# Performance work log

Hardware: AMD Instinct MI355X
Metric: run time of the kernel (lower is better)

Reference implementation:

```python
import jax, jax.numpy as jnp
import numpy as np

B, L, D, H, NL, FF, W, V = 4, 8192, 256, 4, 4, 1024, 512, 14
DH = D // H


def _ln(x, g, b, eps=1e-5):
    m = jnp.mean(x, axis=-1, keepdims=True)
    v = jnp.mean((x - m) ** 2, axis=-1, keepdims=True)
    return (x - m) / jnp.sqrt(v + eps) * g + b


def setup_inputs() -> dict:
    key = jax.random.key(0)
    ks = jax.random.split(key, 12)
    s = 0.02
    inp = {
        "byte_ids": jax.random.randint(ks[0], (B, L), 0, V, dtype=jnp.int32),
        "embed": jax.random.normal(ks[1], (V, D), jnp.float32) * s,
        "wq": jax.random.normal(ks[2], (NL, D, D), jnp.float32) * s,
        "bq": jnp.zeros((NL, D), jnp.float32),
        "wk": jax.random.normal(ks[3], (NL, D, D), jnp.float32) * s,
        "bk": jnp.zeros((NL, D), jnp.float32),
        "wv": jax.random.normal(ks[4], (NL, D, D), jnp.float32) * s,
        "bv": jnp.zeros((NL, D), jnp.float32),
        "wo": jax.random.normal(ks[5], (NL, D, D), jnp.float32) * s,
        "bo": jnp.zeros((NL, D), jnp.float32),
        "ln1_g": jnp.ones((NL, D), jnp.float32),
        "ln1_b": jnp.zeros((NL, D), jnp.float32),
        "ln2_g": jnp.ones((NL, D), jnp.float32),
        "ln2_b": jnp.zeros((NL, D), jnp.float32),
        "w1": jax.random.normal(ks[6], (NL, D, FF), jnp.float32) * s,
        "b1": jnp.zeros((NL, FF), jnp.float32),
        "w2": jax.random.normal(ks[7], (NL, FF, D), jnp.float32) * s,
        "b2": jnp.zeros((NL, D), jnp.float32),
        "lnf_g": jnp.ones((D,), jnp.float32),
        "lnf_b": jnp.zeros((D,), jnp.float32),
        "head_w": jax.random.normal(ks[8], (D, V), jnp.float32) * s,
    }
    return inp


def _forward(byte_ids, embed, wq, bq, wk, bk, wv, bv, wo, bo,
             ln1_g, ln1_b, ln2_g, ln2_b, w1, b1, w2, b2, lnf_g, lnf_b, head_w):
    x = embed[byte_ids]                      # [B, L, D]
    nb = L // W                              # number of 512-wide blocks
    scale = 1.0 / np.sqrt(DH)
    # ALiBi slopes: 2^(-8h/H) for h = 1..H
    slopes = jnp.exp2(-8.0 * jnp.arange(1, H + 1, dtype=jnp.float32) / H)
    qi = jnp.arange(W)[:, None]
    ki = jnp.arange(2 * W)[None, :]
    dist = (W + qi - ki).astype(jnp.float32)            # i - j for kv window [prev, cur]
    base = (dist >= 0) & (dist <= W)                    # causal sliding window (left=512)
    mask = jnp.broadcast_to(base, (nb, W, 2 * W))
    mask = mask.at[0].set(base & (ki >= W))             # first block has no previous block
    bias = -slopes[:, None, None] * dist                # [H, W, 2W]

    for l in range(NL):
        h = _ln(x, ln1_g[l], ln1_b[l])
        q = (h @ wq[l] + bq[l]).reshape(B, nb, W, H, DH)
        k = (h @ wk[l] + bk[l]).reshape(B, nb, W, H, DH)
        v = (h @ wv[l] + bv[l]).reshape(B, nb, W, H, DH)
        kp = jnp.pad(k, ((0, 0), (1, 0), (0, 0), (0, 0), (0, 0)))[:, :nb]
        vp = jnp.pad(v, ((0, 0), (1, 0), (0, 0), (0, 0), (0, 0)))[:, :nb]
        kk = jnp.concatenate([kp, k], axis=2)           # [B, nb, 2W, H, DH]
        vv = jnp.concatenate([vp, v], axis=2)
        s = jnp.einsum('bnqhd,bnkhd->bhnqk', q, kk) * scale + bias[None, :, None]
        s = jnp.where(mask[None, None], s, -1e9)
        p = jax.nn.softmax(s, axis=-1)                  # [B, H, nb, W, 2W]
        o = jnp.einsum('bhnqk,bnkhd->bnqhd', p, vv).reshape(B, L, D)
        x = x + o @ wo[l] + bo[l]
        h2 = _ln(x, ln2_g[l], ln2_b[l])
        x = x + jax.nn.gelu(h2 @ w1[l] + b1[l]) @ w2[l] + b2[l]
    x = _ln(x, lnf_g, lnf_b)
    return x @ head_w                                   # [B, L, V]


def reference(byte_ids, embed, wq, bq, wk, bk, wv, bv, wo, bo,
              ln1_g, ln1_b, ln2_g, ln2_b, w1, b1, w2, b2, lnf_g, lnf_b, head_w):
    return _forward(byte_ids, embed, wq, bq, wk, bk, wv, bv, wo, bo,
                    ln1_g, ln1_b, ln2_g, ln2_b, w1, b1, w2, b2, lnf_g, lnf_b, head_w)
```

## Files before the change

kernel.cpp:

```cpp
#include <hip/hip_runtime.h>

#define NLAYER 4
#define M_TOK 32768

typedef unsigned short u16;
typedef __bf16 bf16x8 __attribute__((ext_vector_type(8)));
typedef float f32x4 __attribute__((ext_vector_type(4)));

__device__ inline float bf2f(u16 u) {
    union { unsigned int i; float f; } x; x.i = ((unsigned int)u) << 16; return x.f;
}
__device__ inline u16 f2bf(float f) {
    union { float f; unsigned int i; } x; x.f = f;
    return (u16)((x.i + 0x8000u) >> 16);
}
__device__ inline bf16x8 ld_frag(const u16* p) {
    union { uint4 u; bf16x8 b; } c; c.u = *(const uint4*)p; return c.b;
}
__device__ inline unsigned pk2(float a, float b) {
    union { float f; unsigned i; } ua, ub; ua.f = a; ub.f = b;
    return __builtin_amdgcn_perm(ub.i + 0x8000u, ua.i + 0x8000u, 0x07060302u);
}
__device__ inline float gelu_f(float x) {
    float z = 0.7978845608028654f * (x + 0.044715f * x * x * x);
    float t = 1.f - 2.f / (__expf(2.f * z) + 1.f);
    return 0.5f * x * (1.f + t);
}
__device__ inline void gload_lds16(const u16* g, u16* l) {
    __builtin_amdgcn_global_load_lds(
        (const __attribute__((address_space(1))) unsigned int*)g,
        (__attribute__((address_space(3))) unsigned int*)l, 16, 0, 0);
}

#define BAR()   asm volatile("s_barrier" ::: "memory")
#define WAIT4() asm volatile("s_waitcnt vmcnt(4)" ::: "memory")
#define WAIT0() asm volatile("s_waitcnt vmcnt(0)" ::: "memory")
#define LGKM0() asm volatile("s_waitcnt lgkmcnt(0)" ::: "memory")

__global__ void sniff_kernel(const u16* __restrict__ raw, int* __restrict__ flag)
{
    if (threadIdx.x == 0 && blockIdx.x == 0) {
        int ok = 1;
        for (int i = 0; i < 32; i++) {
            u16 u = raw[i];
            int e = (u >> 7) & 0xFF;
            if (!(u == 0 || (e >= 90 && e <= 140))) ok = 0;
        }
        *flag = ok;
    }
}

struct IngestArgs { const void* src[20]; int off[21]; };
__global__ __launch_bounds__(256) void ingest_all(
    IngestArgs a, float* __restrict__ dst, const int* __restrict__ flag, int tot)
{
    int gid = blockIdx.x * 256 + threadIdx.x;
    if (gid >= tot) return;
    int lo = 0, hi = 20;
    while (hi - lo > 1) { int mid = (lo + hi) >> 1; if (gid >= a.off[mid]) lo = mid; else hi = mid; }
    int local = gid - a.off[lo];
    if (*flag) dst[gid] = bf2f(((const u16*)a.src[lo])[local]);
    else       dst[gid] = ((const float*)a.src[lo])[local];
}

__global__ __launch_bounds__(256) void pack_qkv(
    const float* __restrict__ wq, const float* __restrict__ wk, const float* __restrict__ wv,
    const float* __restrict__ bq, const float* __restrict__ bk, const float* __restrict__ bv,
    u16* __restrict__ wT, float* __restrict__ bT)
{
    int l = blockIdx.y;
    int idx = blockIdx.x * 256 + threadIdx.x;
    int n = idx >> 8, k = idx & 255;
    const float* w = (n < 256) ? wq : (n < 512) ? wk : wv;
    int nn = n & 255;
    wT[(size_t)l * 768 * 256 + idx] = f2bf(w[(size_t)l * 65536 + k * 256 + nn]);
    if (idx < 768) {
        const float* bb = (idx < 256) ? bq : (idx < 512) ? bk : bv;
        bT[l * 768 + idx] = bb[l * 256 + (idx & 255)];
    }
}

__global__ __launch_bounds__(256) void pack_t(
    const float* __restrict__ src, u16* __restrict__ dst, int R, int C)
{
    int l = blockIdx.y;
    int idx = blockIdx.x * 256 + threadIdx.x;
    int c = idx / R, r = idx % R;
    size_t base = (size_t)l * R * C;
    dst[base + idx] = f2bf(src[base + (size_t)r * C + c]);
}

__global__ __launch_bounds__(256) void embed_kernel(
    const int* __restrict__ ids, const float* __restrict__ emb, float* __restrict__ x)
{
    int t = blockIdx.x * 256 + threadIdx.x;
    int row = t >> 6, c = (t & 63) * 4;
    int id = ids[row];
    float4 e = *(const float4*)(emb + (size_t)id * 256 + c);
    *(float4*)(x + (size_t)row * 256 + c) = e;
}

__global__ __launch_bounds__(256) void ln_kernel(
    const float* __restrict__ x, const float* __restrict__ g, const float* __restrict__ b,
    u16* __restrict__ out)
{
    int row = blockIdx.x * 4 + (threadIdx.x >> 6);
    int lane = threadIdx.x & 63;
    float4 v = *(const float4*)(x + (size_t)row * 256 + lane * 4);
    float s = v.x + v.y + v.z + v.w;
    float s2 = v.x * v.x + v.y * v.y + v.z * v.z + v.w * v.w;
    #pragma unroll
    for (int mk = 1; mk < 64; mk <<= 1) {
        s += __shfl_xor(s, mk, 64);
        s2 += __shfl_xor(s2, mk, 64);
    }
    float mean = s * (1.f / 256.f);
    float var = s2 * (1.f / 256.f) - mean * mean;
    float rstd = rsqrtf(var + 1e-5f);
    int d0 = lane * 4;
    float4 gg = *(const float4*)(g + d0);
    float4 bb = *(const float4*)(b + d0);
    union { unsigned long long u; u16 q[4]; } oo;
    oo.q[0] = f2bf((v.x - mean) * rstd * gg.x + bb.x);
    oo.q[1] = f2bf((v.y - mean) * rstd * gg.y + bb.y);
    oo.q[2] = f2bf((v.z - mean) * rstd * gg.z + bb.z);
    oo.q[3] = f2bf((v.w - mean) * rstd * gg.w + bb.w);
    *(unsigned long long*)(out + (size_t)row * 256 + d0) = oo.u;
}

template <int EPI, int K>
__global__ __launch_bounds__(256, 3) void gemm_db(
    const u16* __restrict__ A, const u16* __restrict__ Bt, const float* __restrict__ bias,
    u16* __restrict__ outB, float* __restrict__ resid, int N)
{
    __shared__ u16 lds[17408];
    constexpr int NC = K / 32;
    int tid = threadIdx.x, lane = tid & 63, wave = tid >> 6;
    int col = lane & 15, quad = lane >> 4;
    int wm = (wave >> 1) * 64, wn = (wave & 1) * 64;
    int bm = blockIdx.x * 128, bn = blockIdx.y * 128;

    u16* A0 = lds;          u16* A1 = lds + 4096;
    u16* B0 = lds + 8192;   u16* B1 = lds + 12288;

    int rL = wave * 32 + (lane >> 2);
    int sx = (lane & 3) ^ ((lane >> 2) & 3);
    const u16* srcA0 = A + (size_t)(bm + rL) * K + sx * 8;
    const u16* srcB0 = Bt + (size_t)(bn + rL) * K + sx * 8;
    int st = wave * 1024 + lane * 8;

    int g8 = (quad ^ (col & 3)) * 8;
    int aoff = (wm + col) * 32 + g8;
    int boff = (wn + col) * 32 + g8;

    f32x4 z4 = { 0.f, 0.f, 0.f, 0.f };
    f32x4 acc[4][4];
    #pragma unroll
    for (int i = 0; i < 4; i++)
        #pragma unroll
        for (int j = 0; j < 4; j++) acc[i][j] = z4;

    #define STAGE(c, Ax, Bx) do {                                        \
        const u16* _a = srcA0 + (c) * 32;                                \
        const u16* _b = srcB0 + (c) * 32;                                \
        gload_lds16(_a, (Ax) + st);                                      \
        gload_lds16(_a + (size_t)16 * K, (Ax) + st + 512);               \
        gload_lds16(_b, (Bx) + st);                                      \
        gload_lds16(_b + (size_t)16 * K, (Bx) + st + 512);               \
    } while (0)

    #define CHUNK(Ax, Bx) do {                                           \
        bf16x8 af[4], bfv[4];                                            \
        _Pragma("unroll")                                                \
        for (int i = 0; i < 4; i++) af[i] = ld_frag((Ax) + aoff + i * 512); \
        _Pragma("unroll")                                                \
        for (int j = 0; j < 4; j++) bfv[j] = ld_frag((Bx) + boff + j * 512); \
        _Pragma("unroll")                                                \
        for (int i = 0; i < 4; i++)                                      \
            _Pragma("unroll")                                            \
            for (int j = 0; j < 4; j++)                                  \
                acc[i][j] = __builtin_amdgcn_mfma_f32_16x16x32_bf16(af[i], bfv[j], acc[i][j], 0, 0, 0); \
    } while (0)

    STAGE(0, A0, B0);
    for (int c = 0; c < NC - 2; c += 2) {
        STAGE(c + 1, A1, B1);
        WAIT4(); BAR();
        CHUNK(A0, B0);
        LGKM0(); BAR();
        STAGE(c + 2, A0, B0);
        WAIT4(); BAR();
        CHUNK(A1, B1);
        LGKM0(); BAR();
    }
    STAGE(NC - 1, A1, B1);
    WAIT4(); BAR();
    CHUNK(A0, B0);
    LGKM0(); BAR();
    WAIT0(); BAR();
    CHUNK(A1, B1);
    __syncthreads();

    if (EPI == 2) {
        float* Cf = (float*)lds;
        #pragma unroll
        for (int h = 0; h < 2; h++) {
            if ((wave & 1) == h) {
                #pragma unroll
                for (int j = 0; j < 4; j++) {
                    float bv = bias[bn + wn + j * 16 + col];
                    #pragma unroll
                    for (int i = 0; i < 4; i++) {
                        int rl = wm + i * 16 + quad * 4;
                        #pragma unroll
                        for (int r = 0; r < 4; r++)
                            Cf[(rl + r) * 68 + j * 16 + col] = acc[i][j][r] + bv;
                    }
                }
            }
            LGKM0(); BAR();
            #pragma unroll
            for (int u = 0; u < 8; u++) {
                int row = u * 16 + (tid >> 4);
                int cseg = (tid & 15) * 4;
                float* rp = resid + (size_t)(bm + row) * N + bn + h * 64 + cseg;
                const float* cp = Cf + row * 68 + cseg;
                float4 rv = *(float4*)rp;
                float4 cv = *(const float4*)cp;
                rv.x += cv.x; rv.y += cv.y; rv.z += cv.z; rv.w += cv.w;
                *(float4*)rp = rv;
            }
            LGKM0(); BAR();
        }
    } else {
        u16* Cs = lds;
        #pragma unroll
        for (int j = 0; j < 4; j++) {
            int ccl = wn + j * 16 + col;
            float bv = bias[bn + ccl];
            #pragma unroll
            for (int i = 0; i < 4; i++) {
                int rl = wm + i * 16 + quad * 4;
                #pragma unroll
                for (int r = 0; r < 4; r++) {
                    float v = acc[i][j][r] + bv;
                    if (EPI == 1) v = gelu_f(v);
                    Cs[(rl + r) * 136 + ccl] = f2bf(v);
                }
            }
        }
        __syncthreads();
        #pragma unroll
        for (int u = 0; u < 8; u++) {
            int row = u * 16 + (tid >> 4);
            int c8 = (tid & 15) * 8;
            u16* op = outB + (size_t)(bm + row) * N + bn + c8;
            *(uint4*)op = *(const uint4*)(Cs + row * 136 + c8);
        }
    }
    #undef STAGE
    #undef CHUNK
}

__global__ __launch_bounds__(512, 2) void mlp2(
    const float* __restrict__ xin, const u16* __restrict__ w1T, const u16* __restrict__ w2T,
    const float* __restrict__ gamma, const float* __restrict__ beta,
    const float* __restrict__ b1, const float* __restrict__ b2, float* __restrict__ xr)
{
    __shared__ u16 L[72704];
    int tid = threadIdx.x, lane = tid & 63, wave = tid >> 6;
    int col = lane & 15, quad = lane >> 4;
    int g8 = (quad ^ (col & 3)) * 8;
    int bm = blockIdx.x * 128;

    {
        int sub = tid & 7, rsel = tid >> 3;
        float4 g4[8], b4[8];
        #pragma unroll
        for (int q = 0; q < 8; q++) {
            g4[q] = *(const float4*)(gamma + sub * 32 + q * 4);
            b4[q] = *(const float4*)(beta  + sub * 32 + q * 4);
        }
        #pragma unroll
        for (int p = 0; p < 2; p++) {
            int row = p * 64 + rsel;
            const float* xp = xin + (size_t)(bm + row) * 256 + sub * 32;
            float4 v4[8];
            #pragma unroll
            for (int q = 0; q < 8; q++) v4[q] = *(const float4*)(xp + q * 4);
            float s1 = 0.f, s2 = 0.f;
            #pragma unroll
            for (int q = 0; q < 8; q++) {
                s1 += v4[q].x + v4[q].y + v4[q].z + v4[q].w;
                s2 += v4[q].x * v4[q].x + v4[q].y * v4[q].y
                    + v4[q].z * v4[q].z + v4[q].w * v4[q].w;
            }
            s1 += __shfl_xor(s1, 1, 64); s2 += __shfl_xor(s2, 1, 64);
            s1 += __shfl_xor(s1, 2, 64); s2 += __shfl_xor(s2, 2, 64);
            s1 += __shfl_xor(s1, 4, 64); s2 += __shfl_xor(s2, 4, 64);
            float mean = s1 * (1.f / 256.f);
            float var  = s2 * (1.f / 256.f) - mean * mean;
            float rstd = rsqrtf(var + 1e-5f);
            #pragma unroll
            for (int j = 0; j < 4; j++) {
                float4 a = v4[2 * j], c = v4[2 * j + 1];
                float4 ga = g4[2 * j], gc = g4[2 * j + 1];
                float4 ba = b4[2 * j], bc = b4[2 * j + 1];
                union { uint4 u; u16 q[8]; } pkv;
                pkv.q[0] = f2bf((a.x - mean) * rstd * ga.x + ba.x);
                pkv.q[1] = f2bf((a.y - mean) * rstd * ga.y + ba.y);
                pkv.q[2] = f2bf((a.z - mean) * rstd * ga.z + ba.z);
                pkv.q[3] = f2bf((a.w - mean) * rstd * ga.w + ba.w);
                pkv.q[4] = f2bf((c.x - mean) * rstd * gc.x + bc.x);
                pkv.q[5] = f2bf((c.y - mean) * rstd * gc.y + bc.y);
                pkv.q[6] = f2bf((c.z - mean) * rstd * gc.z + bc.z);
                pkv.q[7] = f2bf((c.w - mean) * rstd * gc.w + bc.w);
                *(uint4*)(L + sub * 4096 + row * 32 + ((j ^ (row & 3)) * 8)) = pkv.u;
            }
        }
        float2 bv = *(const float2*)(b1 + tid * 2);
        *(float2*)((float*)(L + 70656) + tid * 2) = bv;
    }

    #define STAGE_W1(ff, base) do {                                                  \
        _Pragma("unroll")                                                            \
        for (int gg = 0; gg < 2; gg++) {                                             \
            int u_ = gg * 512 + tid;                                                 \
            int ks_ = u_ >> 7, rowf_ = (u_ & 127) >> 2, s_ = u_ & 3;                 \
            gload_lds16(w1T + (size_t)((ff) * 32 + rowf_) * 256 + ks_ * 32           \
                            + ((s_ ^ (rowf_ & 3)) * 8),                              \
                        L + (base) + u_ * 8);                                        \
        }                                                                            \
    } while (0)

    #define STAGE_W2(ff, base) do {                                                  \
        _Pragma("unroll")                                                            \
        for (int gg = 0; gg < 2; gg++) {                                             \
            int u_ = gg * 512 + tid;                                                 \
            int d_ = u_ >> 2, s_ = u_ & 3;                                           \
            gload_lds16(w2T + (size_t)d_ * 1024 + (ff) * 32 + ((s_ ^ (d_ & 3)) * 8), \
                        L + (base) + u_ * 8);                                        \
        }                                                                            \
    } while (0)

    STAGE_W1(0, 32768);
    STAGE_W2(0, 49152);
    WAIT0(); LGKM0(); BAR();

    f32x4 z4 = { 0.f, 0.f, 0.f, 0.f };
    f32x4 acc2[16];
    #pragma unroll
    for (int n = 0; n < 16; n++) acc2[n] = z4;
    u16* Gw = L + 65536 + wave * 640;
    const float* b1l = (const float*)(L + 70656);
    int aoffB = (wave * 16 + col) * 32 + g8;

    #pragma unroll 2
    for (int f = 0; f < 32; ++f) {
        int pc = f & 1, pn = pc ^ 1;
        if (f < 31) {
            STAGE_W1(f + 1, 32768 + pn * 8192);
            STAGE_W2(f + 1, 49152 + pn * 8192);
            WAIT4();
        } else WAIT0();
        BAR();

        const u16* w1b = L + 32768 + pc * 8192;
        const u16* w2b = L + 49152 + pc * 8192;

        f32x4 a1[2]; a1[0] = z4; a1[1] = z4;
        #pragma unroll
        for (int ks = 0; ks < 8; ks++) {
            bf16x8 hf = ld_frag(L + ks * 4096 + aoffB);
            #pragma unroll
            for (int kt = 0; kt < 2; kt++) {
                bf16x8 wf = ld_frag(w1b + ks * 1024 + (kt * 16 + col) * 32 + g8);
                a1[kt] = __builtin_amdgcn_mfma_f32_16x16x32_bf16(wf, hf, a1[kt], 0, 0, 0);
            }
        }
        #pragma unroll
        for (int kt = 0; kt < 2; kt++) {
            float4 bv = *(const float4*)(b1l + f * 32 + kt * 16 + quad * 4);
            float p0 = gelu_f(a1[kt][0] + bv.x);
            float p1 = gelu_f(a1[kt][1] + bv.y);
            float p2 = gelu_f(a1[kt][2] + bv.z);
            float p3 = gelu_f(a1[kt][3] + bv.w);
            uint2 w; w.x = pk2(p0, p1); w.y = pk2(p2, p3);
            *(uint2*)(Gw + col * 40 + kt * 16 + quad * 4) = w;
        }
        LGKM0();

        bf16x8 gf = ld_frag(Gw + col * 40 + quad * 8);
        #pragma unroll
        for (int nt = 0; nt < 16; nt++) {
            bf16x8 wf2 = ld_frag(w2b + (nt * 16 + col) * 32 + g8);
            acc2[nt] = __builtin_amdgcn_mfma_f32_16x16x32_bf16(gf, wf2, acc2[nt], 0, 0, 0);
        }
        LGKM0(); BAR();
    }

    float b2v[16];
    #pragma unroll
    for (int nt = 0; nt < 16; nt++) b2v[nt] = b2[nt * 16 + col];
    #pragma unroll
    for (int nt = 0; nt < 16; nt++) {
        #pragma unroll
        for (int r = 0; r < 4; r++) {
            float* p = xr + (size_t)(bm + wave * 16 + quad * 4 + r) * 256 + nt * 16 + col;
            *p += acc2[nt][r] + b2v[nt];
        }
    }
    #undef STAGE_W1
    #undef STAGE_W2
}

__global__ __launch_bounds__(256, 3) void attn_kernel(
    const u16* __restrict__ qkv, u16* __restrict__ attno)
{
    __shared__ u16 Ks[64 * 72];
    __shared__ u16 Vt[64 * 68];
    __shared__ u16 Ps[4 * 16 * 72];
    int g = blockIdx.x;
    int xc = g & 7, t = g >> 3;
    int r12 = t & 15, s8 = t >> 4;
    int ng = s8 * 8 + xc;
    int bb = ng >> 4, nn = ng & 15;
    int hh = r12 & 3, t2 = r12 >> 2;
    int tid = threadIdx.x, lane = tid & 63, wave = tid >> 6;
    int q16 = lane & 15, quad = lane >> 4;
    float slope = exp2f(-2.f * (float)(hh + 1));
    float slopeL = slope * 1.44269504f;
    const float C1 = 0.125f * 1.44269504f;

    int qt0 = t2 * 2;
    size_t tok0 = (size_t)bb * 8192 + nn * 512;

    bf16x8 bqf[2][2];
    {
        int qrow = t2 * 128 + wave * 16 + q16;
        const u16* qp = qkv + (tok0 + qrow) * 768 + hh * 64 + quad * 8;
        bqf[0][0] = ld_frag(qp);
        bqf[0][1] = ld_frag(qp + 32);
        const u16* qp1 = qp + (size_t)64 * 768;
        bqf[1][0] = ld_frag(qp1);
        bqf[1][1] = ld_frag(qp1 + 32);
    }

    f32x4 z4 = { 0.f, 0.f, 0.f, 0.f };
    f32x4 oa[2][4];
    #pragma unroll
    for (int s = 0; s < 2; s++)
        #pragma unroll
        for (int dt = 0; dt < 4; dt++) oa[s][dt] = z4;
    float lsum[2] = { 0.f, 0.f };
    u16* Psw = Ps + wave * (16 * 72);

    int c_lo = (nn == 0) ? 8 : qt0;
    int c_hi = qt0 + 9;

    int kkK = tid >> 3, c8k = (tid & 7) * 8;
    int kk2 = (tid & 31) * 2, c8v = (tid >> 5) * 8;

    uint4 pk0, pk1, pv0, pv1;
    auto load_c = [&](int c) {
        int tok = (int)tok0 - 512 + c * 64;
        const u16* bK = qkv + (size_t)(tok + kkK) * 768 + hh * 64 + 256 + c8k;
        pk0 = *(const uint4*)bK;
        pk1 = *(const uint4*)(bK + (size_t)32 * 768);
        const u16* bV = qkv + (size_t)(tok + kk2) * 768 + hh * 64 + 512 + c8v;
        pv0 = *(const uint4*)bV;
        pv1 = *(const uint4*)(bV + 768);
    };
    load_c(c_lo);

    for (int c = c_lo; c <= c_hi; ++c) {
        LGKM0(); BAR();
        *(uint4*)(Ks + kkK * 72 + c8k) = pk0;
        *(uint4*)(Ks + (kkK + 32) * 72 + c8k) = pk1;
        {
            union { uint4 u; u16 s[8]; } a, b;
            a.u = pv0; b.u = pv1;
            #pragma unroll
            for (int j = 0; j < 8; j++) {
                unsigned w = (unsigned)a.s[j] | ((unsigned)b.s[j] << 16);
                *(unsigned*)(Vt + (c8v + j) * 68 + kk2) = w;
            }
        }
        if (c < c_hi) load_c(c + 1);
        LGKM0(); BAR();

        bf16x8 kf[4][2];
        #pragma unroll
        for (int kt = 0; kt < 4; kt++)
            #pragma unroll
            for (int ks = 0; ks < 2; ks++)
                kf[kt][ks] = ld_frag(Ks + (kt * 16 + q16) * 72 + ks * 32 + quad * 8);
        bf16x8 vf[4][2];
        #pragma unroll
        for (int dt = 0; dt < 4; dt++)
            #pragma unroll
            for (int ks = 0; ks < 2; ks++) {
                union { uint2 p[2]; bf16x8 b; } cv;
                const u16* vp = Vt + (dt * 16 + q16) * 68 + ks * 32 + quad * 8;
                cv.p[0] = *(const uint2*)(vp);
                cv.p[1] = *(const uint2*)(vp + 4);
                vf[dt][ks] = cv.b;
            }

        int act0 = (c <= qt0 + 8);
        int act1 = (c >= qt0 + 1);
        #pragma unroll
        for (int s = 0; s < 2; s++) {
            if (s == 0 ? !act0 : !act1) continue;
            f32x4 st[4];
            #pragma unroll
            for (int kt = 0; kt < 4; kt++) {
                f32x4 z = z4;
                #pragma unroll
                for (int ks = 0; ks < 2; ks++)
                    z = __builtin_amdgcn_mfma_f32_16x16x32_bf16(kf[kt][ks], bqf[s][ks], z, 0, 0, 0);
                st[kt] = z;
            }
            int qg = t2 * 128 + s * 64 + wave * 16 + q16;
            int D = 512 + qg - c * 64 - quad * 4;
            float nb = -slopeL * (float)D;
            int qts = qt0 + s;
            int diag = (c == qts) || (c == qts + 8);
            float ls = 0.f;
            #pragma unroll
            for (int kt = 0; kt < 4; kt++) {
                float pk[4];
                #pragma unroll
                for (int r = 0; r < 4; r++) {
                    float bias = fmaf(slopeL, (float)(kt * 16 + r), nb);
                    float p = exp2f(fmaf(st[kt][r], C1, bias));
                    if (diag) {
                        int dd = D - (kt * 16 + r);
                        p = ((unsigned)dd <= 512u) ? p : 0.f;
                    }
                    ls += p; pk[r] = p;
                }
                uint2 w;
                w.x = pk2(pk[0], pk[1]);
                w.y = pk2(pk[2], pk[3]);
                *(uint2*)(Psw + q16 * 72 + kt * 16 + quad * 4) = w;
            }
            lsum[s] += ls;
            bf16x8 pf[2];
            #pragma unroll
            for (int ks = 0; ks < 2; ks++)
                pf[ks] = ld_frag(Psw + q16 * 72 + ks * 32 + quad * 8);
            #pragma unroll
            for (int dt = 0; dt < 4; dt++)
                #pragma unroll
                for (int ks = 0; ks < 2; ks++)
                    oa[s][dt] = __builtin_amdgcn_mfma_f32_16x16x32_bf16(pf[ks], vf[dt][ks], oa[s][dt], 0, 0, 0);
        }
    }

    #pragma unroll
    for (int s = 0; s < 2; s++) {
        float lr = lsum[s];
        lr += __shfl_xor(lr, 16, 64);
        lr += __shfl_xor(lr, 32, 64);
        lsum[s] = lr;
    }
    float* lx = (float*)Psw;
    if (quad == 0) { lx[q16] = lsum[0]; lx[16 + q16] = lsum[1]; }
    #pragma unroll
    for (int s = 0; s < 2; s++) {
        float4 lq = *(const float4*)(lx + s * 16 + quad * 4);
        float inv[4] = { 1.f / lq.x, 1.f / lq.y, 1.f / lq.z, 1.f / lq.w };
        int tokb = (int)tok0 + t2 * 128 + s * 64 + wave * 16 + quad * 4;
        #pragma unroll
        for (int r = 0; r < 4; r++)
            #pragma unroll
            for (int dt = 0; dt < 4; dt++)
                attno[(size_t)(tokb + r) * 256 + hh * 64 + dt * 16 + q16] = f2bf(oa[s][dt][r] * inv[r]);
    }
}

__global__ __launch_bounds__(256) void head_ln_kernel(
    const float* __restrict__ x, const float* __restrict__ g, const float* __restrict__ b,
    const float* __restrict__ hw, const int* __restrict__ flag,
    u16* __restrict__ outb, float* __restrict__ outf)
{
    __shared__ float Wt[14 * 256];
    int tid = threadIdx.x;
    for (int i = tid; i < 14 * 256; i += 256) {
        int v = i >> 8, d = i & 255;
        Wt[i] = hw[d * 14 + v];
    }
    __syncthreads();
    int wave = tid >> 6, lane = tid & 63;
    int row = blockIdx.x * 4 + wave;
    float4 v = *(const float4*)(x + (size_t)row * 256 + lane * 4);
    float s = v.x + v.y + v.z + v.w;
    float s2 = v.x * v.x + v.y * v.y + v.z * v.z + v.w * v.w;
    #pragma unroll
    for (int mk = 1; mk < 64; mk <<= 1) {
        s += __shfl_xor(s, mk, 64);
        s2 += __shfl_xor(s2, mk, 64);
    }
    float mean = s * (1.f / 256.f);
    float var = s2 * (1.f / 256.f) - mean * mean;
    float rstd = rsqrtf(var + 1e-5f);
    int d0 = lane * 4;
    float4 gg = *(const float4*)(g + d0);
    float4 bb = *(const float4*)(b + d0);
    float hv[4];
    hv[0] = (v.x - mean) * rstd * gg.x + bb.x;
    hv[1] = (v.y - mean) * rstd * gg.y + bb.y;
    hv[2] = (v.z - mean) * rstd * gg.z + bb.z;
    hv[3] = (v.w - mean) * rstd * gg.w + bb.w;
    int isbf = *flag;
    for (int vv = 0; vv < 14; vv++) {
        float4 wv4 = *(const float4*)(Wt + vv * 256 + lane * 4);
        float sd = hv[0] * wv4.x + hv[1] * wv4.y + hv[2] * wv4.z + hv[3] * wv4.w;
        #pragma unroll
        for (int mk = 1; mk < 64; mk <<= 1) sd += __shfl_xor(sd, mk, 64);
        if (lane == 0) {
            if (isbf) outb[(size_t)row * 14 + vv] = f2bf(sd);
            else      outf[(size_t)row * 14 + vv] = sd;
        }
    }
}

extern "C" void kernel_launch(void* const* d_in, const int* in_sizes, int n_in,
                              void* d_out, int out_size, void* d_ws, size_t ws_size,
                              hipStream_t stream) {
    (void)out_size; (void)ws_size;
    const int* ids = (const int*)d_in[0];

    char* ws = (char*)d_ws;
    int* flag = (int*)ws; ws += 16;

    IngestArgs ia;
    int off = 0;
    for (int i = 1; i < n_in && i <= 20; i++) {
        ia.src[i - 1] = d_in[i];
        ia.off[i - 1] = off;
        off += in_sizes[i];
    }
    ia.off[20] = off;
    float* fbase = (float*)ws;
    ws += (size_t)((off + 3) & ~3) * 4;
    float* fin[21];
    for (int i = 1; i <= 20; i++) fin[i] = fbase + ia.off[i - 1];

    float* x    = (float*)ws;  ws += (size_t)M_TOK * 256 * 4;
    u16* h      = (u16*)ws;    ws += (size_t)M_TOK * 256 * 2;
    u16* qkv    = (u16*)ws;    ws += (size_t)M_TOK * 768 * 2;
    u16* attno  = (u16*)ws;    ws += (size_t)M_TOK * 256 * 2;
    u16* wqkvT  = (u16*)ws;    ws += (size_t)NLAYER * 768 * 256 * 2;
    u16* woT    = (u16*)ws;    ws += (size_t)NLAYER * 256 * 256 * 2;
    u16* w1T    = (u16*)ws;    ws += (size_t)NLAYER * 1024 * 256 * 2;
    u16* w2T    = (u16*)ws;    ws += (size_t)NLAYER * 256 * 1024 * 2;
    float* bqkv = (float*)ws;  ws += (size_t)NLAYER * 768 * 4;

    sniff_kernel<<<1, 64, 0, stream>>>((const u16*)d_in[1], flag);
    ingest_all<<<(off + 255) / 256, 256, 0, stream>>>(ia, fbase, flag, off);

    pack_qkv<<<dim3(768, NLAYER), 256, 0, stream>>>(fin[2], fin[4], fin[6],
                                                    fin[3], fin[5], fin[7], wqkvT, bqkv);
    pack_t<<<dim3(256, NLAYER), 256, 0, stream>>>(fin[8], woT, 256, 256);
    pack_t<<<dim3(1024, NLAYER), 256, 0, stream>>>(fin[14], w1T, 256, 1024);
    pack_t<<<dim3(1024, NLAYER), 256, 0, stream>>>(fin[16], w2T, 1024, 256);

    embed_kernel<<<8192, 256, 0, stream>>>(ids, fin[1], x);

    for (int l = 0; l < NLAYER; ++l) {
        ln_kernel<<<8192, 256, 0, stream>>>(x, fin[10] + l * 256, fin[11] + l * 256, h);
        gemm_db<0, 256><<<dim3(256, 6), 256, 0, stream>>>(h, wqkvT + (size_t)l * 768 * 256,
                                                          bqkv + l * 768, qkv, nullptr, 768);
        attn_kernel<<<1024, 256, 0, stream>>>(qkv, attno);
        gemm_db<2, 256><<<dim3(256, 2), 256, 0, stream>>>(attno, woT + (size_t)l * 65536,
                                                          fin[9] + l * 256, nullptr, x, 256);
        mlp2<<<256, 512, 0, stream>>>(x, w1T + (size_t)l * 262144,
                                      w2T + (size_t)l * 262144,
                                      fin[12] + l * 256, fin[13] + l * 256,
                                      fin[15] + l * 1024, fin[17] + l * 256, x);
    }
    head_ln_kernel<<<8192, 256, 0, stream>>>(x, fin[18], fin[19], fin[20], flag,
                                             (u16*)d_out, (float*)d_out);
}
```

Before: 1.000 ms.

## Split MLP into producer/consumer waves and fuse next-layer LayerNorm into epilogue

The fused MLP kernel now gives the first four waves the W1 GEMM plus GELU, each over 32 rows. The other four waves run the W2 GEMM one step behind on a double-buffered G tile in LDS, with W2 staging shifted to match. The residual epilogue also computes the next layer's LayerNorm and writes the bf16 h. That removes the standalone ln_kernel launches, and the embed kernel fuses the first LN. The costs are more LDS, more accumulator registers per consumer wave, and idle producer waves during the epilogue.

Result: faster. 978.5 us (-2.2%).

```diff
diff --git a/kernel.cpp b/kernel.cpp
--- a/kernel.cpp
+++ b/kernel.cpp
@@ -34,6 +34,7 @@
 
 #define BAR()   asm volatile("s_barrier" ::: "memory")
 #define WAIT4() asm volatile("s_waitcnt vmcnt(4)" ::: "memory")
+#define WAIT2() asm volatile("s_waitcnt vmcnt(2)" ::: "memory")
 #define WAIT0() asm volatile("s_waitcnt vmcnt(0)" ::: "memory")
 #define LGKM0() asm volatile("s_waitcnt lgkmcnt(0)" ::: "memory")
 
@@ -90,25 +91,18 @@
     dst[base + idx] = f2bf(src[base + (size_t)r * C + c]);
 }
 
-__global__ __launch_bounds__(256) void embed_kernel(
-    const int* __restrict__ ids, const float* __restrict__ emb, float* __restrict__ x)
+__global__ __launch_bounds__(256) void embed_ln(
+    const int* __restrict__ ids, const float* __restrict__ emb,
+    const float* __restrict__ g, const float* __restrict__ b,
+    float* __restrict__ x, u16* __restrict__ h)
 {
     int t = blockIdx.x * 256 + threadIdx.x;
     int row = t >> 6, c = (t & 63) * 4;
     int id = ids[row];
     float4 e = *(const float4*)(emb + (size_t)id * 256 + c);
     *(float4*)(x + (size_t)row * 256 + c) = e;
-}
-
-__global__ __launch_bounds__(256) void ln_kernel(
-    const float* __restrict__ x, const float* __restrict__ g, const float* __restrict__ b,
-    u16* __restrict__ out)
-{
-    int row = blockIdx.x * 4 + (threadIdx.x >> 6);
-    int lane = threadIdx.x & 63;
-    float4 v = *(const float4*)(x + (size_t)row * 256 + lane * 4);
-    float s = v.x + v.y + v.z + v.w;
-    float s2 = v.x * v.x + v.y * v.y + v.z * v.z + v.w * v.w;
+    float s = e.x + e.y + e.z + e.w;
+    float s2 = e.x * e.x + e.y * e.y + e.z * e.z + e.w * e.w;
     #pragma unroll
     for (int mk = 1; mk < 64; mk <<= 1) {
         s += __shfl_xor(s, mk, 64);
@@ -117,15 +111,14 @@
     float mean = s * (1.f / 256.f);
     float var = s2 * (1.f / 256.f) - mean * mean;
     float rstd = rsqrtf(var + 1e-5f);
-    int d0 = lane * 4;
-    float4 gg = *(const float4*)(g + d0);
-    float4 bb = *(const float4*)(b + d0);
+    float4 gg = *(const float4*)(g + c);
+    float4 bb = *(const float4*)(b + c);
     union { unsigned long long u; u16 q[4]; } oo;
-    oo.q[0] = f2bf((v.x - mean) * rstd * gg.x + bb.x);
-    oo.q[1] = f2bf((v.y - mean) * rstd * gg.y + bb.y);
-    oo.q[2] = f2bf((v.z - mean) * rstd * gg.z + bb.z);
-    oo.q[3] = f2bf((v.w - mean) * rstd * gg.w + bb.w);
-    *(unsigned long long*)(out + (size_t)row * 256 + d0) = oo.u;
+    oo.q[0] = f2bf((e.x - mean) * rstd * gg.x + bb.x);
+    oo.q[1] = f2bf((e.y - mean) * rstd * gg.y + bb.y);
+    oo.q[2] = f2bf((e.z - mean) * rstd * gg.z + bb.z);
+    oo.q[3] = f2bf((e.w - mean) * rstd * gg.w + bb.w);
+    *(unsigned long long*)(h + (size_t)row * 256 + c) = oo.u;
 }
 
 template <int EPI, int K>
@@ -262,16 +255,20 @@
     #undef CHUNK
 }
 
-__global__ __launch_bounds__(512, 2) void mlp2(
+template <int FUSE>
+__global__ __launch_bounds__(512, 2) void mlp2s(
     const float* __restrict__ xin, const u16* __restrict__ w1T, const u16* __restrict__ w2T,
     const float* __restrict__ gamma, const float* __restrict__ beta,
-    const float* __restrict__ b1, const float* __restrict__ b2, float* __restrict__ xr)
-{
-    __shared__ u16 L[72704];
+    const float* __restrict__ b1, const float* __restrict__ b2, float* __restrict__ xr,
+    const float* __restrict__ g1n, const float* __restrict__ b1n, u16* __restrict__ hout)
+{
+    __shared__ u16 L[77824];
     int tid = threadIdx.x, lane = tid & 63, wave = tid >> 6;
     int col = lane & 15, quad = lane >> 4;
     int g8 = (quad ^ (col & 3)) * 8;
     int bm = blockIdx.x * 128;
+    int isProd = (wave < 4);
+    int pw = wave & 3;
 
     {
         int sub = tid & 7, rsel = tid >> 3;
@@ -319,7 +316,7 @@
             }
         }
         float2 bv = *(const float2*)(b1 + tid * 2);
-        *(float2*)((float*)(L + 70656) + tid * 2) = bv;
+        *(float2*)((float*)(L + 75776) + tid * 2) = bv;
     }
 
     #define STAGE_W1(ff, base) do {                                                  \
@@ -344,70 +341,122 @@
     } while (0)
 
     STAGE_W1(0, 32768);
-    STAGE_W2(0, 49152);
     WAIT0(); LGKM0(); BAR();
 
     f32x4 z4 = { 0.f, 0.f, 0.f, 0.f };
-    f32x4 acc2[16];
+    f32x4 acc2[2][16];
     #pragma unroll
-    for (int n = 0; n < 16; n++) acc2[n] = z4;
-    u16* Gw = L + 65536 + wave * 640;
-    const float* b1l = (const float*)(L + 70656);
-    int aoffB = (wave * 16 + col) * 32 + g8;
+    for (int mt = 0; mt < 2; mt++)
+        #pragma unroll
+        for (int nt = 0; nt < 16; nt++) acc2[mt][nt] = z4;
+    const float* b1l = (const float*)(L + 75776);
 
     #pragma unroll 2
     for (int f = 0; f < 32; ++f) {
         int pc = f & 1, pn = pc ^ 1;
-        if (f < 31) {
-            STAGE_W1(f + 1, 32768 + pn * 8192);
-            STAGE_W2(f + 1, 49152 + pn * 8192);
-            WAIT4();
-        } else WAIT0();
+        if (f < 31) STAGE_W1(f + 1, 32768 + pn * 8192);
+        STAGE_W2(f, 49152 + pc * 8192);
+        if (f == 31) WAIT2(); else WAIT4();
         BAR();
 
-        const u16* w1b = L + 32768 + pc * 8192;
-        const u16* w2b = L + 49152 + pc * 8192;
-
-        f32x4 a1[2]; a1[0] = z4; a1[1] = z4;
-        #pragma unroll
-        for (int ks = 0; ks < 8; ks++) {
-            bf16x8 hf = ld_frag(L + ks * 4096 + aoffB);
-            #pragma unroll
-            for (int kt = 0; kt < 2; kt++) {
-                bf16x8 wf = ld_frag(w1b + ks * 1024 + (kt * 16 + col) * 32 + g8);
-                a1[kt] = __builtin_amdgcn_mfma_f32_16x16x32_bf16(wf, hf, a1[kt], 0, 0, 0);
-            }
-        }
-        #pragma unroll
-        for (int kt = 0; kt < 2; kt++) {
-            float4 bv = *(const float4*)(b1l + f * 32 + kt * 16 + quad * 4);
-            float p0 = gelu_f(a1[kt][0] + bv.x);
-            float p1 = gelu_f(a1[kt][1] + bv.y);
-            float p2 = gelu_f(a1[kt][2] + bv.z);
-            float p3 = gelu_f(a1[kt][3] + bv.w);
-            uint2 w; w.x = pk2(p0, p1); w.y = pk2(p2, p3);
-            *(uint2*)(Gw + col * 40 + kt * 16 + quad * 4) = w;
-        }
-        LGKM0();
-
-        bf16x8 gf = ld_frag(Gw + col * 40 + quad * 8);
+        if (isProd) {
+            const u16* w1b = L + 32768 + pc * 8192;
+            f32x4 a1[2][2];
+            a1[0][0] = z4; a1[0][1] = z4; a1[1][0] = z4; a1[1][1] = z4;
+            #pragma unroll
+            for (int ks = 0; ks < 8; ks++) {
+                bf16x8 hf0 = ld_frag(L + ks * 4096 + (pw * 32 + col) * 32 + g8);
+                bf16x8 hf1 = ld_frag(L + ks * 4096 + (pw * 32 + 16 + col) * 32 + g8);
+                #pragma unroll
+                for (int kt = 0; kt < 2; kt++) {
+                    bf16x8 wf = ld_frag(w1b + ks * 1024 + (kt * 16 + col) * 32 + g8);
+                    a1[0][kt] = __builtin_amdgcn_mfma_f32_16x16x32_bf16(wf, hf0, a1[0][kt], 0, 0, 0);
+                    a1[1][kt] = __builtin_amdgcn_mfma_f32_16x16x32_bf16(wf, hf1, a1[1][kt], 0, 0, 0);
+                }
+            }
+            u16* gd = L + 65536 + pc * 5120;
+            #pragma unroll
+            for (int mt = 0; mt < 2; mt++)
+                #pragma unroll
+                for (int kt = 0; kt < 2; kt++) {
+                    float4 bv = *(const float4*)(b1l + f * 32 + kt * 16 + quad * 4);
+                    float p0 = gelu_f(a1[mt][kt][0] + bv.x);
+                    float p1 = gelu_f(a1[mt][kt][1] + bv.y);
+                    float p2 = gelu_f(a1[mt][kt][2] + bv.z);
+                    float p3 = gelu_f(a1[mt][kt][3] + bv.w);
+                    uint2 w; w.x = pk2(p0, p1); w.y = pk2(p2, p3);
+                    *(uint2*)(gd + (pw * 32 + mt * 16 + col) * 40 + kt * 16 + quad * 4) = w;
+                }
+        } else if (f > 0) {
+            const u16* gs = L + 65536 + pn * 5120;
+            const u16* w2b = L + 49152 + pn * 8192;
+            bf16x8 gf0 = ld_frag(gs + (pw * 32 + col) * 40 + quad * 8);
+            bf16x8 gf1 = ld_frag(gs + (pw * 32 + 16 + col) * 40 + quad * 8);
+            #pragma unroll
+            for (int nt = 0; nt < 16; nt++) {
+                bf16x8 wf2 = ld_frag(w2b + (nt * 16 + col) * 32 + g8);
+                acc2[0][nt] = __builtin_amdgcn_mfma_f32_16x16x32_bf16(gf0, wf2, acc2[0][nt], 0, 0, 0);
+                acc2[1][nt] = __builtin_amdgcn_mfma_f32_16x16x32_bf16(gf1, wf2, acc2[1][nt], 0, 0, 0);
+            }
+        }
+        LGKM0(); BAR();
+    }
+
+    WAIT0();
+    if (!isProd) {
+        const u16* gs = L + 65536 + 5120;
+        const u16* w2b = L + 49152 + 8192;
+        bf16x8 gf0 = ld_frag(gs + (pw * 32 + col) * 40 + quad * 8);
+        bf16x8 gf1 = ld_frag(gs + (pw * 32 + 16 + col) * 40 + quad * 8);
         #pragma unroll
         for (int nt = 0; nt < 16; nt++) {
             bf16x8 wf2 = ld_frag(w2b + (nt * 16 + col) * 32 + g8);
-            acc2[nt] = __builtin_amdgcn_mfma_f32_16x16x32_bf16(gf, wf2, acc2[nt], 0, 0, 0);
-        }
+            acc2[0][nt] = __builtin_amdgcn_mfma_f32_16x16x32_bf16(gf0, wf2, acc2[0][nt], 0, 0, 0);
+            acc2[1][nt] = __builtin_amdgcn_mfma_f32_16x16x32_bf16(gf1, wf2, acc2[1][nt], 0, 0, 0);
+        }
+
+        float b2v[16], g1v[16], b1v[16];
+        #pragma unroll
+        for (int nt = 0; nt < 16; nt++) {
+            b2v[nt] = b2[nt * 16 + col];
+            if (FUSE) { g1v[nt] = g1n[nt * 16 + col]; b1v[nt] = b1n[nt * 16 + col]; }
+        }
+        #pragma unroll
+        for (int mt = 0; mt < 2; mt++)
+            #pragma unroll
+            for (int r = 0; r < 4; r++) {
+                int m = pw * 32 + mt * 16 + quad * 4 + r;
+                float* xrow = xr + (size_t)(bm + m) * 256;
+                float s1 = 0.f, s2 = 0.f;
+                #pragma unroll
+                for (int nt = 0; nt < 16; nt++) {
+                    float xv = xrow[nt * 16 + col] + acc2[mt][nt][r] + b2v[nt];
+                    acc2[mt][nt][r] = xv;
+                    s1 += xv; s2 += xv * xv;
+                }
+                #pragma unroll
+                for (int nt = 0; nt < 16; nt++) xrow[nt * 16 + col] = acc2[mt][nt][r];
+                if (FUSE) {
+                    s1 += __shfl_xor(s1, 1, 64); s2 += __shfl_xor(s2, 1, 64);
+                    s1 += __shfl_xor(s1, 2, 64); s2 += __shfl_xor(s2, 2, 64);
+                    s1 += __shfl_xor(s1, 4, 64); s2 += __shfl_xor(s2, 4, 64);
+                    s1 += __shfl_xor(s1, 8, 64); s2 += __shfl_xor(s2, 8, 64);
+                    float mean = s1 * (1.f / 256.f);
+                    float var  = s2 * (1.f / 256.f) - mean * mean;
+                    float rstd = rsqrtf(var + 1e-5f);
+                    #pragma unroll
+                    for (int nt = 0; nt < 16; nt++)
+                        L[m * 256 + nt * 16 + col] =
+                            f2bf((acc2[mt][nt][r] - mean) * rstd * g1v[nt] + b1v[nt]);
+                }
+            }
+    }
+    if (FUSE) {
         LGKM0(); BAR();
-    }
-
-    float b2v[16];
-    #pragma unroll
-    for (int nt = 0; nt < 16; nt++) b2v[nt] = b2[nt * 16 + col];
-    #pragma unroll
-    for (int nt = 0; nt < 16; nt++) {
-        #pragma unroll
-        for (int r = 0; r < 4; r++) {
-            float* p = xr + (size_t)(bm + wave * 16 + quad * 4 + r) * 256 + nt * 16 + col;
-            *p += acc2[nt][r] + b2v[nt];
+        #pragma unroll
+        for (int i = 0; i < 8; i++) {
+            int flat = i * 4096 + tid * 8;
+            *(uint4*)(hout + (size_t)bm * 256 + flat) = *(const uint4*)(L + flat);
         }
     }
     #undef STAGE_W1
@@ -667,19 +716,27 @@
     pack_t<<<dim3(1024, NLAYER), 256, 0, stream>>>(fin[14], w1T, 256, 1024);
     pack_t<<<dim3(1024, NLAYER), 256, 0, stream>>>(fin[16], w2T, 1024, 256);
 
-    embed_kernel<<<8192, 256, 0, stream>>>(ids, fin[1], x);
+    embed_ln<<<8192, 256, 0, stream>>>(ids, fin[1], fin[10], fin[11], x, h);
 
     for (int l = 0; l < NLAYER; ++l) {
-        ln_kernel<<<8192, 256, 0, stream>>>(x, fin[10] + l * 256, fin[11] + l * 256, h);
         gemm_db<0, 256><<<dim3(256, 6), 256, 0, stream>>>(h, wqkvT + (size_t)l * 768 * 256,
                                                           bqkv + l * 768, qkv, nullptr, 768);
         attn_kernel<<<1024, 256, 0, stream>>>(qkv, attno);
         gemm_db<2, 256><<<dim3(256, 2), 256, 0, stream>>>(attno, woT + (size_t)l * 65536,
                                                           fin[9] + l * 256, nullptr, x, 256);
-        mlp2<<<256, 512, 0, stream>>>(x, w1T + (size_t)l * 262144,
-                                      w2T + (size_t)l * 262144,
-                                      fin[12] + l * 256, fin[13] + l * 256,
-                                      fin[15] + l * 1024, fin[17] + l * 256, x);
+        if (l < NLAYER - 1) {
+            mlp2s<1><<<256, 512, 0, stream>>>(x, w1T + (size_t)l * 262144,
+                                              w2T + (size_t)l * 262144,
+                                              fin[12] + l * 256, fin[13] + l * 256,
+                                              fin[15] + l * 1024, fin[17] + l * 256, x,
+                                              fin[10] + (l + 1) * 256, fin[11] + (l + 1) * 256, h);
+        } else {
+            mlp2s<0><<<256, 512, 0, stream>>>(x, w1T + (size_t)l * 262144,
+                                              w2T + (size_t)l * 262144,
+                                              fin[12] + l * 256, fin[13] + l * 256,
+                                              fin[15] + l * 1024, fin[17] + l * 256, x,
+                                              fin[10], fin[11], h);
+        }
     }
     head_ln_kernel<<<8192, 256, 0, stream>>>(x, fin[18], fin[19], fin[20], flag,
                                              (u16*)d_out, (float*)d_out);
```
